# Performance work log

Hardware: AMD Instinct MI355X
Metric: run time of the kernel (lower is better)

## Reference

```python
import jax, jax.numpy as jnp
import numpy as np

EPS = 1e-8


def _l2_normalize(x, eps=EPS):
    n = jnp.linalg.norm(x, axis=-1, keepdims=True)
    return x / jnp.maximum(n, eps)


def setup_inputs() -> dict:
    key = jax.random.key(0)
    k1, k2, k3 = jax.random.split(key, 3)
    N_s, N_q, D, C = 65536, 131072, 256, 512
    return {
        "support_features": jax.random.normal(k1, (N_s, D), dtype=jnp.float32),
        "support_labels": jax.random.randint(k2, (N_s,), 0, C, dtype=jnp.int64),
        "query_features": jax.random.normal(k3, (N_q, D), dtype=jnp.float32),
        "logit_scale": jnp.asarray(5.0, dtype=jnp.float32),
        "proto_shrink": jnp.asarray(-2.0, dtype=jnp.float32),
        "num_classes": C,
    }


def reference(support_features, support_labels, query_features, logit_scale, proto_shrink, num_classes):
    # L2-normalize features
    s = _l2_normalize(support_features)            # [N_s, D]
    q = _l2_normalize(query_features)              # [N_q, D]

    labels = support_labels.astype(jnp.int32)
    # per-class segment mean (replaces the python unique/mask loop)
    sums = jax.ops.segment_sum(s, labels, num_segments=num_classes)        # [C, D]
    counts = jax.ops.segment_sum(jnp.ones((s.shape[0],), s.dtype), labels,
                                 num_segments=num_classes)                 # [C]
    counts = jnp.maximum(counts, 1.0)
    class_means = sums / counts[:, None]                                   # [C, D]

    global_centroid = jnp.mean(s, axis=0, keepdims=True)                    # [1, D]

    alpha_base = jnp.clip(jax.nn.sigmoid(proto_shrink), 0.0, 0.4)
    alpha = (alpha_base / jnp.sqrt(counts))[:, None]                        # [C, 1]
    prototypes = (1.0 - alpha) * class_means + alpha * global_centroid
    prototypes = _l2_normalize(prototypes)                                  # [C, D]

    scale = jnp.clip(logit_scale, 1.0, 100.0)
    logits = q @ prototypes.T * scale                                       # [N_q, C]
    unique_classes = jnp.arange(num_classes, dtype=jnp.int32)
    return logits, unique_classes
```

## Files before the change

kernel.cpp:

```cpp
#include <hip/hip_runtime.h>

typedef __attribute__((ext_vector_type(4)))  float f32x4;
typedef __attribute__((ext_vector_type(16))) float f32x16;
typedef __attribute__((ext_vector_type(8)))  short short8;

#define DD 256
#define CC 512
#define LDP 264

__device__ __forceinline__ unsigned short f2bf(float f) {
    union { float f; unsigned u; } x; x.f = f;
    unsigned r = x.u + 0x7FFFu + ((x.u >> 16) & 1u);
    return (unsigned short)(r >> 16);
}

__device__ __forceinline__ f32x4 ntload4(const f32x4* p) {
    return __builtin_nontemporal_load(p);
}

__global__ __launch_bounds__(256) void class_sum_kernel(
    const f32x4* __restrict__ S, const int* __restrict__ labels,
    float* __restrict__ sums2, float* __restrict__ counts2, int N_s)
{
    const int c = blockIdx.x >> 1, half = blockIdx.x & 1;
    const int w = threadIdx.x >> 6, l = threadIdx.x & 63;
    const int seg  = N_s >> 3;
    const int base = half * (N_s >> 1) + w * seg;
    const int4* lab4 = (const int4*)(labels + base);
    const int iters = seg >> 8;

    float ax = 0.f, ay = 0.f, az = 0.f, aw = 0.f;
    int cnt = 0;

    int4 p0v = lab4[l];
    int4 p1v = (iters > 1) ? lab4[64 + l] : make_int4(-1, -1, -1, -1);

    for (int it = 0; it < iters; ++it) {
        int4 lv = p0v;
        p0v = p1v;
        p1v = (it + 2 < iters) ? lab4[(it + 2) * 64 + l] : make_int4(-1, -1, -1, -1);
        #pragma unroll
        for (int s = 0; s < 4; ++s) {
            int lab = (s == 0) ? lv.x : (s == 1) ? lv.y : (s == 2) ? lv.z : lv.w;
            unsigned long long m = __ballot(lab == c);
            cnt += __popcll(m);
            while (m) {
                int p0 = __ffsll((long long)m) - 1; m &= m - 1;
                int p1 = -1;
                if (m) { p1 = __ffsll((long long)m) - 1; m &= m - 1; }
                int row0 = base + (it * 64 + p0) * 4 + s;
                f32x4 v0 = ntload4(&S[(size_t)row0 * 64 + l]);
                f32x4 v1 = {0.f, 0.f, 0.f, 0.f};
                if (p1 >= 0) {
                    int row1 = base + (it * 64 + p1) * 4 + s;
                    v1 = ntload4(&S[(size_t)row1 * 64 + l]);
                }
                float ss0 = v0[0]*v0[0] + v0[1]*v0[1] + v0[2]*v0[2] + v0[3]*v0[3];
                float ss1 = v1[0]*v1[0] + v1[1]*v1[1] + v1[2]*v1[2] + v1[3]*v1[3];
                #pragma unroll
                for (int off = 32; off; off >>= 1) {
                    ss0 += __shfl_xor(ss0, off);
                    ss1 += __shfl_xor(ss1, off);
                }
                float inv0 = 1.0f / fmaxf(sqrtf(ss0), 1e-8f);
                ax += v0[0]*inv0; ay += v0[1]*inv0; az += v0[2]*inv0; aw += v0[3]*inv0;
                if (p1 >= 0) {
                    float inv1 = 1.0f / fmaxf(sqrtf(ss1), 1e-8f);
                    ax += v1[0]*inv1; ay += v1[1]*inv1; az += v1[2]*inv1; aw += v1[3]*inv1;
                }
            }
        }
    }

    __shared__ float lred[4][DD];
    __shared__ float lcnt[4];
    lred[w][4*l+0] = ax; lred[w][4*l+1] = ay; lred[w][4*l+2] = az; lred[w][4*l+3] = aw;
    if (l == 0) lcnt[w] = (float)cnt;
    __syncthreads();
    int t = threadIdx.x;
    sums2[(size_t)(half * CC + c) * DD + t] = lred[0][t] + lred[1][t] + lred[2][t] + lred[3][t];
    if (t == 0) counts2[half * CC + c] = lcnt[0] + lcnt[1] + lcnt[2] + lcnt[3];
}

__global__ __launch_bounds__(256) void centroid_kernel(
    const float* __restrict__ sums2, float* __restrict__ gpart)
{
    const int d = threadIdx.x, b = blockIdx.x;
    float s = 0.f;
    for (int j = 0; j < 64; ++j) {
        int c = b * 64 + j;
        s += sums2[(size_t)c * DD + d] + sums2[(size_t)(CC + c) * DD + d];
    }
    gpart[b * DD + d] = s;
}

__global__ __launch_bounds__(256) void proto_kernel(
    const float* __restrict__ sums2, const float* __restrict__ counts2,
    const float* __restrict__ gpart, const float* __restrict__ proto_shrink,
    unsigned short* __restrict__ Pbf, float* __restrict__ outUC, int N_s)
{
    const int c = blockIdx.x, d = threadIdx.x;
    float ps = proto_shrink[0];
    float ab = 1.0f / (1.0f + __expf(-ps));
    ab = fminf(fmaxf(ab, 0.0f), 0.4f);

    float sum  = sums2[(size_t)c * DD + d] + sums2[(size_t)(CC + c) * DD + d];
    float cntv = fmaxf(counts2[c] + counts2[CC + c], 1.0f);
    float g = 0.f;
    #pragma unroll
    for (int b = 0; b < 8; ++b) g += gpart[b * DD + d];
    g /= (float)N_s;

    float mean  = sum / cntv;
    float alpha = ab / sqrtf(cntv);
    float p = (1.0f - alpha) * mean + alpha * g;

    float ss = p * p;
    #pragma unroll
    for (int off = 32; off; off >>= 1) ss += __shfl_xor(ss, off);
    __shared__ float l4[4];
    if ((threadIdx.x & 63) == 0) l4[threadIdx.x >> 6] = ss;
    __syncthreads();
    ss = l4[0] + l4[1] + l4[2] + l4[3];
    float inv = 1.0f / fmaxf(sqrtf(ss), 1e-8f);
    Pbf[(size_t)c * DD + d] = f2bf(p * inv);
    if (d == 0) outUC[c] = (float)c;
}

__global__ __launch_bounds__(256) void logits_kernel(
    const float4* __restrict__ Q, const unsigned short* __restrict__ Pbf,
    const float* __restrict__ logit_scale, float* __restrict__ out)
{
    __shared__ unsigned short smem[128 * LDP];
    unsigned short* bufA = smem;
    unsigned short* buf0 = smem;
    unsigned short* buf1 = smem + 64 * LDP;

    const int t  = threadIdx.x;
    const int m0 = blockIdx.x * 128;
    const int br = t >> 2, bq = t & 3;
    const unsigned short* Pb = Pbf + (size_t)br * DD + bq * 64;

    short8 breg[8];
    #pragma unroll
    for (int i = 0; i < 8; ++i) breg[i] = *(const short8*)(Pb + i * 8);

    #pragma unroll
    for (int pass = 0; pass < 2; ++pass) {
        const int r = pass * 64 + (t >> 2), q4 = t & 3;
        const float4* qrow = Q + (size_t)(m0 + r) * 64;
        float4 v[16];
        #pragma unroll
        for (int i = 0; i < 16; ++i) v[i] = qrow[q4 * 16 + i];
        float ss = 0.f;
        #pragma unroll
        for (int i = 0; i < 16; ++i) ss += v[i].x*v[i].x + v[i].y*v[i].y + v[i].z*v[i].z + v[i].w*v[i].w;
        ss += __shfl_xor(ss, 1); ss += __shfl_xor(ss, 2);
        float inv = 1.0f / fmaxf(sqrtf(ss), 1e-8f);
        unsigned short* dst = &bufA[r * LDP + q4 * 64];
        #pragma unroll
        for (int i = 0; i < 8; ++i) {
            short8 pk;
            float4 a0 = v[2*i], b0 = v[2*i+1];
            pk[0] = (short)f2bf(a0.x*inv); pk[1] = (short)f2bf(a0.y*inv);
            pk[2] = (short)f2bf(a0.z*inv); pk[3] = (short)f2bf(a0.w*inv);
            pk[4] = (short)f2bf(b0.x*inv); pk[5] = (short)f2bf(b0.y*inv);
            pk[6] = (short)f2bf(b0.z*inv); pk[7] = (short)f2bf(b0.w*inv);
            *(short8*)(dst + i * 8) = pk;
        }
    }
    __builtin_amdgcn_sched_barrier(0);
    asm volatile("s_waitcnt lgkmcnt(0)");
    __builtin_amdgcn_sched_barrier(0);
    __builtin_amdgcn_s_barrier();
    __builtin_amdgcn_sched_barrier(0);

    const int w = t >> 6, l = t & 63;
    const int arow = 32 * w + (l & 31);
    const int kgrp = (l >> 5) * 8;
    short8 a[16];
    #pragma unroll
    for (int k = 0; k < 16; ++k)
        a[k] = *(const short8*)(&bufA[arow * LDP + k * 16 + kgrp]);
    __builtin_amdgcn_sched_barrier(0);
    asm volatile("s_waitcnt lgkmcnt(0)");
    __builtin_amdgcn_sched_barrier(0);
    __builtin_amdgcn_s_barrier();
    __builtin_amdgcn_sched_barrier(0);

    {
        unsigned short* dst = &buf0[br * LDP + bq * 64];
        #pragma unroll
        for (int i = 0; i < 8; ++i) *(short8*)(dst + i * 8) = breg[i];
        const unsigned short* src = Pb + (size_t)64 * DD;
        #pragma unroll
        for (int i = 0; i < 8; ++i) breg[i] = *(const short8*)(src + i * 8);
    }
    __builtin_amdgcn_sched_barrier(0);
    asm volatile("s_waitcnt lgkmcnt(0)");
    __builtin_amdgcn_sched_barrier(0);
    __builtin_amdgcn_s_barrier();
    __builtin_amdgcn_sched_barrier(0);

    const float s = fminf(fmaxf(logit_scale[0], 1.0f), 100.0f);

    unsigned short* bufR = buf0;
    unsigned short* bufW = buf1;

    for (int c0 = 0; c0 < 8; ++c0) {
        if (c0 < 7) {
            unsigned short* dst = &bufW[br * LDP + bq * 64];
            #pragma unroll
            for (int i = 0; i < 8; ++i) *(short8*)(dst + i * 8) = breg[i];
        }
        if (c0 < 6) {
            const unsigned short* src = Pb + (size_t)(c0 + 2) * 64 * DD;
            #pragma unroll
            for (int i = 0; i < 8; ++i) breg[i] = *(const short8*)(src + i * 8);
        }
        const int n0 = c0 * 64;
        #pragma unroll
        for (int nf = 0; nf < 2; ++nf) {
            f32x16 acc;
            #pragma unroll
            for (int r = 0; r < 16; ++r) acc[r] = 0.f;
            const unsigned short* bbase = &bufR[(nf * 32 + (l & 31)) * LDP + kgrp];
            __builtin_amdgcn_s_setprio(1);
            #pragma unroll
            for (int k = 0; k < 16; ++k) {
                short8 b = *(const short8*)(bbase + k * 16);
                acc = __builtin_amdgcn_mfma_f32_32x32x16_bf16(a[k], b, acc, 0, 0, 0);
            }
            __builtin_amdgcn_s_setprio(0);
            const int col   = n0 + nf * 32 + (l & 31);
            const int rbase = m0 + 32 * w + 4 * (l >> 5);
            #pragma unroll
            for (int r = 0; r < 16; ++r) {
                int row = rbase + (r & 3) + 8 * (r >> 2);
                __builtin_nontemporal_store(acc[r] * s, &out[(size_t)row * CC + col]);
            }
        }
        if (c0 < 7) {
            __builtin_amdgcn_sched_barrier(0);
            asm volatile("s_waitcnt lgkmcnt(0)");
            __builtin_amdgcn_sched_barrier(0);
            __builtin_amdgcn_s_barrier();
            __builtin_amdgcn_sched_barrier(0);
            unsigned short* tmp = bufR; bufR = bufW; bufW = tmp;
        }
    }
}

extern "C" void kernel_launch(void* const* d_in, const int* in_sizes, int n_in,
                              void* d_out, int out_size, void* d_ws, size_t ws_size,
                              hipStream_t stream) {
    const float* S      = (const float*)d_in[0];
    const int*   labels = (const int*)d_in[1];
    const float* Qf     = (const float*)d_in[2];
    const float* lscale = (const float*)d_in[3];
    const float* pshr   = (const float*)d_in[4];

    const int N_s = in_sizes[0] / DD;
    const int N_q = in_sizes[2] / DD;

    float* sums2         = (float*)d_ws;
    float* counts2       = (float*)((char*)d_ws + 1048576);
    float* gpart         = (float*)((char*)d_ws + 1052672);
    unsigned short* Pbf  = (unsigned short*)((char*)d_ws + 1060864);

    float* out   = (float*)d_out;
    float* outUC = out + (size_t)N_q * CC;

    class_sum_kernel<<<2 * CC, 256, 0, stream>>>((const f32x4*)S, labels, sums2, counts2, N_s);
    centroid_kernel<<<8, 256, 0, stream>>>(sums2, gpart);
    proto_kernel<<<CC, 256, 0, stream>>>(sums2, counts2, gpart, pshr, Pbf, outUC, N_s);
    logits_kernel<<<N_q / 128, 256, 0, stream>>>((const float4*)Qf, Pbf, lscale, out);
}
```

Before: 120.7 us.

## Load query fragments straight into registers and double rows per block

The logits kernel now reads query rows directly from global memory into MFMA A-fragment registers, with no LDS staging. Normalization is deferred by scaling the accumulator output with per-row inverse norms gathered through shuffles. Each block now covers 256 rows, so every B tile in LDS feeds two MFMA chains, and launch bounds request 2 blocks per CU. The class-sum kernel also batches up to four matching support rows per ballot loop to expose more memory parallelism. Risks are higher register pressure from 32 A fragments, and bf16 rounding now applied to unnormalized query values.

```diff
diff --git a/kernel.cpp b/kernel.cpp
--- a/kernel.cpp
+++ b/kernel.cpp
@@ -32,13 +32,13 @@
     float ax = 0.f, ay = 0.f, az = 0.f, aw = 0.f;
     int cnt = 0;
 
-    int4 p0v = lab4[l];
-    int4 p1v = (iters > 1) ? lab4[64 + l] : make_int4(-1, -1, -1, -1);
+    int4 pf0 = lab4[l];
+    int4 pf1 = (iters > 1) ? lab4[64 + l] : make_int4(-1, -1, -1, -1);
 
     for (int it = 0; it < iters; ++it) {
-        int4 lv = p0v;
-        p0v = p1v;
-        p1v = (it + 2 < iters) ? lab4[(it + 2) * 64 + l] : make_int4(-1, -1, -1, -1);
+        int4 lv = pf0;
+        pf0 = pf1;
+        pf1 = (it + 2 < iters) ? lab4[(it + 2) * 64 + l] : make_int4(-1, -1, -1, -1);
         #pragma unroll
         for (int s = 0; s < 4; ++s) {
             int lab = (s == 0) ? lv.x : (s == 1) ? lv.y : (s == 2) ? lv.z : lv.w;
@@ -46,28 +46,34 @@
             cnt += __popcll(m);
             while (m) {
                 int p0 = __ffsll((long long)m) - 1; m &= m - 1;
-                int p1 = -1;
-                if (m) { p1 = __ffsll((long long)m) - 1; m &= m - 1; }
-                int row0 = base + (it * 64 + p0) * 4 + s;
-                f32x4 v0 = ntload4(&S[(size_t)row0 * 64 + l]);
-                f32x4 v1 = {0.f, 0.f, 0.f, 0.f};
-                if (p1 >= 0) {
-                    int row1 = base + (it * 64 + p1) * 4 + s;
-                    v1 = ntload4(&S[(size_t)row1 * 64 + l]);
-                }
-                float ss0 = v0[0]*v0[0] + v0[1]*v0[1] + v0[2]*v0[2] + v0[3]*v0[3];
-                float ss1 = v1[0]*v1[0] + v1[1]*v1[1] + v1[2]*v1[2] + v1[3]*v1[3];
+                int p1 = -1, p2 = -1, p3 = -1;
+                if (m) { p1 = __ffsll((long long)m) - 1; m &= m - 1;
+                    if (m) { p2 = __ffsll((long long)m) - 1; m &= m - 1;
+                        if (m) { p3 = __ffsll((long long)m) - 1; m &= m - 1; } } }
+                f32x4 v0 = ntload4(&S[(size_t)(base + (it * 64 + p0) * 4 + s) * 64 + l]);
+                f32x4 v1 = {0,0,0,0}, v2 = {0,0,0,0}, v3 = {0,0,0,0};
+                if (p1 >= 0) v1 = ntload4(&S[(size_t)(base + (it * 64 + p1) * 4 + s) * 64 + l]);
+                if (p2 >= 0) v2 = ntload4(&S[(size_t)(base + (it * 64 + p2) * 4 + s) * 64 + l]);
+                if (p3 >= 0) v3 = ntload4(&S[(size_t)(base + (it * 64 + p3) * 4 + s) * 64 + l]);
+                float s0 = v0[0]*v0[0] + v0[1]*v0[1] + v0[2]*v0[2] + v0[3]*v0[3];
+                float s1 = v1[0]*v1[0] + v1[1]*v1[1] + v1[2]*v1[2] + v1[3]*v1[3];
+                float s2 = v2[0]*v2[0] + v2[1]*v2[1] + v2[2]*v2[2] + v2[3]*v2[3];
+                float s3 = v3[0]*v3[0] + v3[1]*v3[1] + v3[2]*v3[2] + v3[3]*v3[3];
                 #pragma unroll
                 for (int off = 32; off; off >>= 1) {
-                    ss0 += __shfl_xor(ss0, off);
-                    ss1 += __shfl_xor(ss1, off);
+                    s0 += __shfl_xor(s0, off);
+                    s1 += __shfl_xor(s1, off);
+                    s2 += __shfl_xor(s2, off);
+                    s3 += __shfl_xor(s3, off);
                 }
-                float inv0 = 1.0f / fmaxf(sqrtf(ss0), 1e-8f);
-                ax += v0[0]*inv0; ay += v0[1]*inv0; az += v0[2]*inv0; aw += v0[3]*inv0;
-                if (p1 >= 0) {
-                    float inv1 = 1.0f / fmaxf(sqrtf(ss1), 1e-8f);
-                    ax += v1[0]*inv1; ay += v1[1]*inv1; az += v1[2]*inv1; aw += v1[3]*inv1;
-                }
+                float i0 = 1.0f / fmaxf(sqrtf(s0), 1e-8f);
+                ax += v0[0]*i0; ay += v0[1]*i0; az += v0[2]*i0; aw += v0[3]*i0;
+                if (p1 >= 0) { float i1 = 1.0f / fmaxf(sqrtf(s1), 1e-8f);
+                    ax += v1[0]*i1; ay += v1[1]*i1; az += v1[2]*i1; aw += v1[3]*i1; }
+                if (p2 >= 0) { float i2 = 1.0f / fmaxf(sqrtf(s2), 1e-8f);
+                    ax += v2[0]*i2; ay += v2[1]*i2; az += v2[2]*i2; aw += v2[3]*i2; }
+                if (p3 >= 0) { float i3 = 1.0f / fmaxf(sqrtf(s3), 1e-8f);
+                    ax += v3[0]*i3; ay += v3[1]*i3; az += v3[2]*i3; aw += v3[3]*i3; }
             }
         }
     }
@@ -127,17 +133,16 @@
     if (d == 0) outUC[c] = (float)c;
 }
 
-__global__ __launch_bounds__(256) void logits_kernel(
+__global__ __launch_bounds__(256, 2) void logits_kernel(
     const float4* __restrict__ Q, const unsigned short* __restrict__ Pbf,
     const float* __restrict__ logit_scale, float* __restrict__ out)
 {
-    __shared__ unsigned short smem[128 * LDP];
-    unsigned short* bufA = smem;
-    unsigned short* buf0 = smem;
-    unsigned short* buf1 = smem + 64 * LDP;
+    __shared__ unsigned short Blds[2][64 * LDP];
 
     const int t  = threadIdx.x;
-    const int m0 = blockIdx.x * 128;
+    const int w  = t >> 6, l = t & 63;
+    const int lr = l & 31, lh = l >> 5;
+    const int m0 = blockIdx.x * 256;
     const int br = t >> 2, bq = t & 3;
     const unsigned short* Pb = Pbf + (size_t)br * DD + bq * 64;
 
@@ -145,29 +150,47 @@
     #pragma unroll
     for (int i = 0; i < 8; ++i) breg[i] = *(const short8*)(Pb + i * 8);
 
-    #pragma unroll
-    for (int pass = 0; pass < 2; ++pass) {
-        const int r = pass * 64 + (t >> 2), q4 = t & 3;
-        const float4* qrow = Q + (size_t)(m0 + r) * 64;
-        float4 v[16];
-        #pragma unroll
-        for (int i = 0; i < 16; ++i) v[i] = qrow[q4 * 16 + i];
+    short8 a0[16], a1[16];
+    float inv0, inv1;
+    #pragma unroll
+    for (int rb = 0; rb < 2; ++rb) {
+        const int row = m0 + 64 * w + rb * 32 + lr;
+        const float4* qr = Q + (size_t)row * 64 + lh * 2;
         float ss = 0.f;
         #pragma unroll
-        for (int i = 0; i < 16; ++i) ss += v[i].x*v[i].x + v[i].y*v[i].y + v[i].z*v[i].z + v[i].w*v[i].w;
-        ss += __shfl_xor(ss, 1); ss += __shfl_xor(ss, 2);
+        for (int k = 0; k < 16; ++k) {
+            float4 x = qr[k * 4];
+            float4 y = qr[k * 4 + 1];
+            ss += x.x*x.x + x.y*x.y + x.z*x.z + x.w*x.w
+                + y.x*y.x + y.y*y.y + y.z*y.z + y.w*y.w;
+            short8 f;
+            f[0] = (short)f2bf(x.x); f[1] = (short)f2bf(x.y);
+            f[2] = (short)f2bf(x.z); f[3] = (short)f2bf(x.w);
+            f[4] = (short)f2bf(y.x); f[5] = (short)f2bf(y.y);
+            f[6] = (short)f2bf(y.z); f[7] = (short)f2bf(y.w);
+            if (rb == 0) a0[k] = f; else a1[k] = f;
+        }
+        ss += __shfl_xor(ss, 32);
         float inv = 1.0f / fmaxf(sqrtf(ss), 1e-8f);
-        unsigned short* dst = &bufA[r * LDP + q4 * 64];
-        #pragma unroll
-        for (int i = 0; i < 8; ++i) {
-            short8 pk;
-            float4 a0 = v[2*i], b0 = v[2*i+1];
-            pk[0] = (short)f2bf(a0.x*inv); pk[1] = (short)f2bf(a0.y*inv);
-            pk[2] = (short)f2bf(a0.z*inv); pk[3] = (short)f2bf(a0.w*inv);
-            pk[4] = (short)f2bf(b0.x*inv); pk[5] = (short)f2bf(b0.y*inv);
-            pk[6] = (short)f2bf(b0.z*inv); pk[7] = (short)f2bf(b0.w*inv);
-            *(short8*)(dst + i * 8) = pk;
-        }
+        if (rb == 0) inv0 = inv; else inv1 = inv;
+    }
+
+    const float s = fminf(fmaxf(logit_scale[0], 1.0f), 100.0f);
+    float sv0[16], sv1[16];
+    #pragma unroll
+    for (int r = 0; r < 16; ++r) {
+        int src = (r & 3) + 8 * (r >> 2) + 4 * lh;
+        sv0[r] = __shfl(inv0, src) * s;
+        sv1[r] = __shfl(inv1, src) * s;
+    }
+
+    {
+        unsigned short* dst = &Blds[0][br * LDP + bq * 64];
+        #pragma unroll
+        for (int i = 0; i < 8; ++i) *(short8*)(dst + i * 8) = breg[i];
+        const unsigned short* src = Pb + (size_t)64 * DD;
+        #pragma unroll
+        for (int i = 0; i < 8; ++i) breg[i] = *(const short8*)(src + i * 8);
     }
     __builtin_amdgcn_sched_barrier(0);
     asm volatile("s_waitcnt lgkmcnt(0)");
@@ -175,41 +198,9 @@
     __builtin_amdgcn_s_barrier();
     __builtin_amdgcn_sched_barrier(0);
 
-    const int w = t >> 6, l = t & 63;
-    const int arow = 32 * w + (l & 31);
-    const int kgrp = (l >> 5) * 8;
-    short8 a[16];
-    #pragma unroll
-    for (int k = 0; k < 16; ++k)
-        a[k] = *(const short8*)(&bufA[arow * LDP + k * 16 + kgrp]);
-    __builtin_amdgcn_sched_barrier(0);
-    asm volatile("s_waitcnt lgkmcnt(0)");
-    __builtin_amdgcn_sched_barrier(0);
-    __builtin_amdgcn_s_barrier();
-    __builtin_amdgcn_sched_barrier(0);
-
-    {
-        unsigned short* dst = &buf0[br * LDP + bq * 64];
-        #pragma unroll
-        for (int i = 0; i < 8; ++i) *(short8*)(dst + i * 8) = breg[i];
-        const unsigned short* src = Pb + (size_t)64 * DD;
-        #pragma unroll
-        for (int i = 0; i < 8; ++i) breg[i] = *(const short8*)(src + i * 8);
-    }
-    __builtin_amdgcn_sched_barrier(0);
-    asm volatile("s_waitcnt lgkmcnt(0)");
-    __builtin_amdgcn_sched_barrier(0);
-    __builtin_amdgcn_s_barrier();
-    __builtin_amdgcn_sched_barrier(0);
-
-    const float s = fminf(fmaxf(logit_scale[0], 1.0f), 100.0f);
-
-    unsigned short* bufR = buf0;
-    unsigned short* bufW = buf1;
-
     for (int c0 = 0; c0 < 8; ++c0) {
         if (c0 < 7) {
-            unsigned short* dst = &bufW[br * LDP + bq * 64];
+            unsigned short* dst = &Blds[(c0 + 1) & 1][br * LDP + bq * 64];
             #pragma unroll
             for (int i = 0; i < 8; ++i) *(short8*)(dst + i * 8) = breg[i];
         }
@@ -218,26 +209,27 @@
             #pragma unroll
             for (int i = 0; i < 8; ++i) breg[i] = *(const short8*)(src + i * 8);
         }
-        const int n0 = c0 * 64;
         #pragma unroll
         for (int nf = 0; nf < 2; ++nf) {
-            f32x16 acc;
-            #pragma unroll
-            for (int r = 0; r < 16; ++r) acc[r] = 0.f;
-            const unsigned short* bbase = &bufR[(nf * 32 + (l & 31)) * LDP + kgrp];
+            f32x16 acc0, acc1;
+            #pragma unroll
+            for (int r = 0; r < 16; ++r) { acc0[r] = 0.f; acc1[r] = 0.f; }
+            const unsigned short* bbase = &Blds[c0 & 1][(nf * 32 + lr) * LDP + lh * 8];
             __builtin_amdgcn_s_setprio(1);
             #pragma unroll
             for (int k = 0; k < 16; ++k) {
                 short8 b = *(const short8*)(bbase + k * 16);
-                acc = __builtin_amdgcn_mfma_f32_32x32x16_bf16(a[k], b, acc, 0, 0, 0);
+                acc0 = __builtin_amdgcn_mfma_f32_32x32x16_bf16(a0[k], b, acc0, 0, 0, 0);
+                acc1 = __builtin_amdgcn_mfma_f32_32x32x16_bf16(a1[k], b, acc1, 0, 0, 0);
             }
             __builtin_amdgcn_s_setprio(0);
-            const int col   = n0 + nf * 32 + (l & 31);
-            const int rbase = m0 + 32 * w + 4 * (l >> 5);
+            const int col   = c0 * 64 + nf * 32 + lr;
+            const int rbase = m0 + 64 * w + 4 * lh;
             #pragma unroll
             for (int r = 0; r < 16; ++r) {
                 int row = rbase + (r & 3) + 8 * (r >> 2);
-                __builtin_nontemporal_store(acc[r] * s, &out[(size_t)row * CC + col]);
+                __builtin_nontemporal_store(acc0[r] * sv0[r], &out[(size_t)row * CC + col]);
+                __builtin_nontemporal_store(acc1[r] * sv1[r], &out[(size_t)(row + 32) * CC + col]);
             }
         }
         if (c0 < 7) {
@@ -246,7 +238,6 @@
             __builtin_amdgcn_sched_barrier(0);
             __builtin_amdgcn_s_barrier();
             __builtin_amdgcn_sched_barrier(0);
-            unsigned short* tmp = bufR; bufR = bufW; bufW = tmp;
         }
     }
 }
@@ -274,5 +265,5 @@
     class_sum_kernel<<<2 * CC, 256, 0, stream>>>((const f32x4*)S, labels, sums2, counts2, N_s);
     centroid_kernel<<<8, 256, 0, stream>>>(sums2, gpart);
     proto_kernel<<<CC, 256, 0, stream>>>(sums2, counts2, gpart, pshr, Pbf, outUC, N_s);
-    logits_kernel<<<N_q / 128, 256, 0, stream>>>((const float4*)Qf, Pbf, lscale, out);
-}
+    logits_kernel<<<N_q / 256, 256, 0, stream>>>((const float4*)Qf, Pbf, lscale, out);
+}
```

After: 201.7 us. 67.1% more time.
